# Optimization experiments

Measured on AMD Instinct MI355X. Metric: run time of the kernel, lower is better.

The kernel has to match this reference:

```python
import jax, jax.numpy as jnp
import numpy as np

B, L, D = 32, 256, 1024
ALIGN = 1024
FF = 2048
NUM_CLASSES = 3


def setup_inputs() -> dict:
    key = jax.random.key(0)
    ks = jax.random.split(key, 10)
    u = lambda k, shape: jax.random.uniform(k, shape, jnp.float32, -1.0, 1.0)
    return {
        "premises": jax.random.normal(ks[0], (B, L, D), jnp.float32),
        "hypotheses": jax.random.normal(ks[1], (B, L, D), jnp.float32),
        "W_F": u(ks[2], (D, ALIGN)),
        "W_G": u(ks[3], (2 * D, FF)),
        "W1": u(ks[4], (2 * FF, FF)) * 0.02,
        "b1": jnp.zeros((FF,), jnp.float32),
        "W2": u(ks[5], (FF, FF)) * 0.02,
        "b2": jnp.zeros((FF,), jnp.float32),
        "W3": u(ks[6], (FF, NUM_CLASSES)) * 0.02,
        "b3": jnp.zeros((NUM_CLASSES,), jnp.float32),
    }


def reference(premises, hypotheses, W_F, W_G, W1, b1, W2, b2, W3, b3):
    # ---- align: tanh-projected cross attention ----
    F_p = jnp.tanh(jnp.einsum("bpd,da->bpa", premises, W_F))      # [B,Lp,A]
    F_h = jnp.tanh(jnp.einsum("bhd,da->bha", hypotheses, W_F))    # [B,Lh,A]
    eijs = jnp.einsum("bpa,bha->bph", F_p, F_h)                   # [B,Lp,Lh]
    attn = jax.nn.softmax(eijs, axis=-1)                          # tf.nn.softmax: last axis
    betas = jnp.einsum("bph,bhd->bpd", attn, hypotheses)          # [B,Lp,D]
    alphas = jnp.einsum("bph,bpd->bhd", attn, premises)           # [B,Lh,D]

    # ---- compare (dropout is identity: p_keep = 1.0 at eval) ----
    V1 = jnp.tanh(jnp.concatenate([premises, betas], axis=2) @ W_G)    # [B,Lp,FF]
    V2 = jnp.tanh(jnp.concatenate([hypotheses, alphas], axis=2) @ W_G) # [B,Lh,FF]

    # ---- aggregate: sum-pool over sequence, concat ----
    agg = jnp.concatenate([V1.sum(axis=1), V2.sum(axis=1)], axis=1)    # [B,2*FF]

    # ---- classifier MLP ----
    a1 = jnp.tanh(agg @ W1 + b1)
    a2 = jnp.tanh(a1 @ W2 + b2)
    logits = a2 @ W3 + b3                                              # [B,3]
    return logits
```

## Files before the change

### kernel.cpp

```cpp
#include <hip/hip_runtime.h>
#include <hip/hip_bf16.h>
#include <stdint.h>


typedef __attribute__((ext_vector_type(8))) short    short8_t;
typedef __attribute__((ext_vector_type(4))) float    float4_t;
typedef __attribute__((ext_vector_type(8))) _Float16 half8_t;
typedef __attribute__((ext_vector_type(4))) _Float16 half4_t;

#define DEVI static __device__ __forceinline__

DEVI short f2bf(float f) {
  union { float f; unsigned u; } v; v.f = f;
  unsigned r = v.u + 0x7fffu + ((v.u >> 16) & 1u);
  return (short)(r >> 16);
}
DEVI float bf2f(short s) {
  union { unsigned u; float f; } v;
  v.u = ((unsigned)(unsigned short)s) << 16;
  return v.f;
}
DEVI void split2(float x, short& hi, short& lo) {
  hi = f2bf(x);
  lo = f2bf(x - bf2f(hi));
}
DEVI float fast_tanh(float x) {
  float e = __expf(2.0f * x);
  return 1.0f - 2.0f / (e + 1.0f);
}
DEVI void gload16(const void* g, void* l) {
  __builtin_amdgcn_global_load_lds(
      (const __attribute__((address_space(1))) void*)g,
      (__attribute__((address_space(3))) void*)l, 16, 0, 0);
}

template <int DO_TANH, int OUT_MODE>
__global__ __launch_bounds__(256) void gemm_nt_split(
    const short* __restrict__ Ah, const short* __restrict__ Al, int lda, long sA,
    const short* __restrict__ Bh, const short* __restrict__ Bl, int ldb, long sB,
    void* __restrict__ Ch, void* __restrict__ Cl, int ldc, long sC,
    int M, int K, int kslices)
{
  __shared__ __align__(16) short Ash[128][40];
  __shared__ __align__(16) short Asl[128][40];
  __shared__ __align__(16) short Bsh[128][40];
  __shared__ __align__(16) short Bsl[128][40];

  const int z  = blockIdx.z;
  const int zb = z / kslices;
  const int zk = z - zb * kslices;
  const int Ksub = K / kslices;
  const int kbeg = zk * Ksub, kend = kbeg + Ksub;

  Ah += (size_t)zb * sA;  Al += (size_t)zb * sA;
  Bh += (size_t)zb * sB;  Bl += (size_t)zb * sB;

  const int row0 = blockIdx.x * 128;
  const int col0 = blockIdx.y * 128;

  const int t    = threadIdx.x;
  const int lane = t & 63;
  const int wave = t >> 6;
  const int wr = wave >> 1, wc = wave & 1;
  const int m15 = lane & 15, q = lane >> 4;

  float4_t acc[4][4];
#pragma unroll
  for (int i = 0; i < 4; ++i)
#pragma unroll
    for (int j = 0; j < 4; ++j) acc[i][j] = (float4_t)0.0f;

  for (int k0 = kbeg; k0 < kend; k0 += 32) {
#pragma unroll
    for (int i = 0; i < 2; ++i) {
      int c  = t + 256 * i;
      int r  = c >> 2;
      int kc = (c & 3) << 3;
      size_t ao = (size_t)(row0 + r) * lda + k0 + kc;
      size_t bo = (size_t)(col0 + r) * ldb + k0 + kc;
      *(int4*)(&Ash[r][kc]) = *(const int4*)(Ah + ao);
      *(int4*)(&Asl[r][kc]) = *(const int4*)(Al + ao);
      *(int4*)(&Bsh[r][kc]) = *(const int4*)(Bh + bo);
      *(int4*)(&Bsl[r][kc]) = *(const int4*)(Bl + bo);
    }
    __syncthreads();

    short8_t ah[4], al[4];
#pragma unroll
    for (int i = 0; i < 4; ++i) {
      ah[i] = *(const short8_t*)(&Ash[wr * 64 + i * 16 + m15][q * 8]);
      al[i] = *(const short8_t*)(&Asl[wr * 64 + i * 16 + m15][q * 8]);
    }
#pragma unroll
    for (int j = 0; j < 4; ++j) {
      short8_t bh = *(const short8_t*)(&Bsh[wc * 64 + j * 16 + m15][q * 8]);
      short8_t bl = *(const short8_t*)(&Bsl[wc * 64 + j * 16 + m15][q * 8]);
#pragma unroll
      for (int i = 0; i < 4; ++i) {
        acc[i][j] = __builtin_amdgcn_mfma_f32_16x16x32_bf16(ah[i], bh, acc[i][j], 0, 0, 0);
        acc[i][j] = __builtin_amdgcn_mfma_f32_16x16x32_bf16(ah[i], bl, acc[i][j], 0, 0, 0);
        acc[i][j] = __builtin_amdgcn_mfma_f32_16x16x32_bf16(al[i], bh, acc[i][j], 0, 0, 0);
      }
    }
    __syncthreads();
  }

  short* Chs = (short*)Ch + (size_t)zb * sC;
  short* Cls = (short*)Cl + (size_t)zb * sC;
  float* Cf  = (float*)Ch + (size_t)zb * sC;
#pragma unroll
  for (int i = 0; i < 4; ++i) {
#pragma unroll
    for (int r = 0; r < 4; ++r) {
      int gm = row0 + wr * 64 + i * 16 + q * 4 + r;
      if (gm < M) {
#pragma unroll
        for (int j = 0; j < 4; ++j) {
          int gn = col0 + wc * 64 + j * 16 + m15;
          float v = acc[i][j][r];
          if (DO_TANH) v = fast_tanh(v);
          if (OUT_MODE == 0) {
            atomicAdd(&Cf[(size_t)gm * ldc + gn], v);
          } else {
            short hi, lo; split2(v, hi, lo);
            Chs[(size_t)gm * ldc + gn] = hi;
            Cls[(size_t)gm * ldc + gn] = lo;
          }
        }
      }
    }
  }
}

template <int MODE>
__global__ __launch_bounds__(256) void gemm_f16(
    const _Float16* __restrict__ A, int lda, long sA,
    const _Float16* __restrict__ B, int ldb, long sB,
    _Float16* __restrict__ C, int ldc, long sC,
    int K, float* __restrict__ agg)
{
  __shared__ __align__(16) _Float16 As[2 * 128 * 32];
  __shared__ __align__(16) _Float16 Bs[2 * 128 * 32];

  const int z = blockIdx.z;
  A += (size_t)z * sA;
  B += (size_t)z * sB;

  const int row0 = blockIdx.x * 128;
  const int col0 = blockIdx.y * 128;
  const int t = threadIdx.x, lane = t & 63, wave = t >> 6;
  const int wr = wave >> 1, wc = wave & 1;
  const int m15 = lane & 15, q = lane >> 4;

  const int srow = wave * 32 + (lane >> 2);
  const int cg   = ((lane & 3) ^ ((lane >> 3) & 3)) * 8;
  const _Float16* gA0 = A + (size_t)(row0 + srow) * lda + cg;
  const _Float16* gA1 = gA0 + (size_t)16 * lda;
  const _Float16* gB0 = B + (size_t)(col0 + srow) * ldb + cg;
  const _Float16* gB1 = gB0 + (size_t)16 * ldb;
  const _Float16* gA0b = gA0 + 32;
  const _Float16* gA1b = gA1 + 32;
  const _Float16* gB0b = gB0 + 32;
  const _Float16* gB1b = gB1 + 32;
  _Float16* lA0  = &As[(wave * 32) * 32];
  _Float16* lA1  = &As[(wave * 32 + 16) * 32];
  _Float16* lB0  = &Bs[(wave * 32) * 32];
  _Float16* lB1  = &Bs[(wave * 32 + 16) * 32];
  _Float16* lA0b = lA0 + 4096;
  _Float16* lA1b = lA1 + 4096;
  _Float16* lB0b = lB0 + 4096;
  _Float16* lB1b = lB1 + 4096;

  const int fs = (q ^ ((m15 >> 1) & 3)) * 8;
  int aoff[4], boff[4];
#pragma unroll
  for (int i = 0; i < 4; ++i) {
    aoff[i] = (wr * 64 + i * 16 + m15) * 32 + fs;
    boff[i] = (wc * 64 + i * 16 + m15) * 32 + fs;
  }

  float4_t acc[4][4];
#pragma unroll
  for (int i = 0; i < 4; ++i)
#pragma unroll
    for (int j = 0; j < 4; ++j) acc[i][j] = (float4_t)0.0f;

  for (int k0 = 0; k0 < K; k0 += 64) {
    gload16(gA0, lA0);  gload16(gA1, lA1);
    gload16(gB0, lB0);  gload16(gB1, lB1);
    gload16(gA0b, lA0b); gload16(gA1b, lA1b);
    gload16(gB0b, lB0b); gload16(gB1b, lB1b);
    gA0 += 64; gA1 += 64; gB0 += 64; gB1 += 64;
    gA0b += 64; gA1b += 64; gB0b += 64; gB1b += 64;
    __syncthreads();

#pragma unroll
    for (int h = 0; h < 2; ++h) {
      half8_t af[4], bfr[4];
#pragma unroll
      for (int i = 0; i < 4; ++i) af[i]  = *(const half8_t*)&As[h * 4096 + aoff[i]];
#pragma unroll
      for (int j = 0; j < 4; ++j) bfr[j] = *(const half8_t*)&Bs[h * 4096 + boff[j]];
#pragma unroll
      for (int i = 0; i < 4; ++i)
#pragma unroll
        for (int j = 0; j < 4; ++j)
          acc[i][j] = __builtin_amdgcn_mfma_f32_16x16x32_f16(af[i], bfr[j], acc[i][j], 0, 0, 0);
    }
    __syncthreads();
  }

  if (MODE == 2) {
    const int half_ = row0 >= 8192;
    const int b     = (row0 & 8191) >> 8;
#pragma unroll
    for (int j = 0; j < 4; ++j) {
      float s = 0.0f;
#pragma unroll
      for (int i = 0; i < 4; ++i)
#pragma unroll
        for (int r = 0; r < 4; ++r) s += fast_tanh(acc[i][j][r]);
      s += __shfl_xor(s, 16);
      s += __shfl_xor(s, 32);
      if (q == 0) {
        int col = col0 + wc * 64 + j * 16 + m15;
        atomicAdd(&agg[(size_t)b * 4096 + half_ * 2048 + col], s);
      }
    }
  } else {
    _Float16* Cp = C + (size_t)z * sC;
#pragma unroll
    for (int i = 0; i < 4; ++i)
#pragma unroll
      for (int r = 0; r < 4; ++r) {
        int gm = row0 + wr * 64 + i * 16 + q * 4 + r;
#pragma unroll
        for (int j = 0; j < 4; ++j) {
          int gn = col0 + wc * 64 + j * 16 + m15;
          Cp[(size_t)gm * ldc + gn] = (_Float16)acc[i][j][r];
        }
      }
  }
}

__global__ __launch_bounds__(256) void transpose_split(
    const float* __restrict__ in, short* __restrict__ oh, short* __restrict__ ol,
    int R, int C)
{
  __shared__ float tile[32][33];
  const int tx = threadIdx.x & 31, ty = threadIdx.x >> 5;
  const int c0 = blockIdx.x * 32, r0 = blockIdx.y * 32;
#pragma unroll
  for (int i = 0; i < 4; ++i) {
    int r = ty + i * 8;
    tile[r][tx] = in[(size_t)(r0 + r) * C + c0 + tx];
  }
  __syncthreads();
#pragma unroll
  for (int i = 0; i < 4; ++i) {
    int cc = ty + i * 8;
    float v = tile[tx][cc];
    short hi, lo; split2(v, hi, lo);
    size_t o = (size_t)(c0 + cc) * R + r0 + tx;
    oh[o] = hi;
    ol[o] = lo;
  }
}

__global__ __launch_bounds__(256) void transpose_f16(
    const float* __restrict__ in, _Float16* __restrict__ out, int R, int C)
{
  __shared__ float tile[32][33];
  const int tx = threadIdx.x & 31, ty = threadIdx.x >> 5;
  const int c0 = blockIdx.x * 32, r0 = blockIdx.y * 32;
#pragma unroll
  for (int i = 0; i < 4; ++i) {
    int r = ty + i * 8;
    tile[r][tx] = in[(size_t)(r0 + r) * C + c0 + tx];
  }
  __syncthreads();
#pragma unroll
  for (int i = 0; i < 4; ++i) {
    int cc = ty + i * 8;
    out[(size_t)(c0 + cc) * R + r0 + tx] = (_Float16)tile[tx][cc];
  }
}

__global__ __launch_bounds__(256) void transpose_f16_ph(
    const float* __restrict__ P, const float* __restrict__ Hh,
    _Float16* __restrict__ out)
{
  __shared__ float tile[32][33];
  const int zz = blockIdx.z;
  const float* in = (zz < 32 ? P : Hh) + (size_t)(zz & 31) * (256 * 1024);
  _Float16* o = out + (size_t)zz * (1024 * 256);
  const int tx = threadIdx.x & 31, ty = threadIdx.x >> 5;
  const int c0 = blockIdx.x * 32, r0 = blockIdx.y * 32;
#pragma unroll
  for (int i = 0; i < 4; ++i) {
    int r = ty + i * 8;
    tile[r][tx] = in[(size_t)(r0 + r) * 1024 + c0 + tx];
  }
  __syncthreads();
#pragma unroll
  for (int i = 0; i < 4; ++i) {
    int cc = ty + i * 8;
    o[(size_t)(c0 + cc) * 256 + r0 + tx] = (_Float16)tile[tx][cc];
  }
}

__global__ __launch_bounds__(256) void transpose_b2b(
    const short* __restrict__ in, short* __restrict__ out,
    int R, int C, long sIn, long sOut)
{
  __shared__ short tile[32][33];
  in  += (size_t)blockIdx.z * sIn;
  out += (size_t)blockIdx.z * sOut;
  const int tx = threadIdx.x & 31, ty = threadIdx.x >> 5;
  const int c0 = blockIdx.x * 32, r0 = blockIdx.y * 32;
#pragma unroll
  for (int i = 0; i < 4; ++i) {
    int r = ty + i * 8;
    tile[r][tx] = in[(size_t)(r0 + r) * C + c0 + tx];
  }
  __syncthreads();
#pragma unroll
  for (int i = 0; i < 4; ++i) {
    int cc = ty + i * 8;
    out[(size_t)(c0 + cc) * R + r0 + tx] = tile[tx][cc];
  }
}

__global__ __launch_bounds__(256) void conv_in(
    const float* __restrict__ P, const float* __restrict__ Hh,
    short* __restrict__ oh, short* __restrict__ ol, _Float16* __restrict__ cat)
{
  const int zz = blockIdx.z;
  const float* in = zz ? Hh : P;
  oh  += (size_t)zz * 8192 * 1024;
  ol  += (size_t)zz * 8192 * 1024;
  cat += (size_t)zz * 8192 * 2048;
  size_t i = ((size_t)blockIdx.x * 256 + threadIdx.x) * 4;
  float4 v = *(const float4*)&in[i];
  short4 h, l;
  split2(v.x, h.x, l.x); split2(v.y, h.y, l.y);
  split2(v.z, h.z, l.z); split2(v.w, h.w, l.w);
  *(short4*)&oh[i] = h;
  *(short4*)&ol[i] = l;
  size_t row = i >> 10;
  int col    = (int)(i & 1023);
  half4_t c16;
  c16.x = (_Float16)v.x; c16.y = (_Float16)v.y;
  c16.z = (_Float16)v.z; c16.w = (_Float16)v.w;
  *(half4_t*)&cat[row * 2048 + col] = c16;
}

__global__ __launch_bounds__(256) void conv_split(
    const float* __restrict__ in, short* __restrict__ oh, short* __restrict__ ol,
    int n)
{
  int i = (blockIdx.x * 256 + threadIdx.x) * 4;
  if (i < n) {
    float4 v = *(const float4*)&in[i];
    short4 h, l;
    split2(v.x, h.x, l.x); split2(v.y, h.y, l.y);
    split2(v.z, h.z, l.z); split2(v.w, h.w, l.w);
    *(short4*)&oh[i] = h;
    *(short4*)&ol[i] = l;
  }
}

__global__ __launch_bounds__(256) void zero_f32(float* __restrict__ p, int n)
{
  int i = blockIdx.x * 256 + threadIdx.x;
  if (i < n) p[i] = 0.0f;
}

__global__ __launch_bounds__(256) void softmax_rows(
    const float* __restrict__ e, _Float16* __restrict__ attn)
{
  const int row  = blockIdx.x * 4 + (threadIdx.x >> 6);
  const int lane = threadIdx.x & 63;
  const float4 v = *(const float4*)&e[(size_t)row * 256 + lane * 4];
  float m = fmaxf(fmaxf(v.x, v.y), fmaxf(v.z, v.w));
#pragma unroll
  for (int off = 32; off; off >>= 1) m = fmaxf(m, __shfl_xor(m, off));
  float e0 = __expf(v.x - m), e1 = __expf(v.y - m);
  float e2 = __expf(v.z - m), e3 = __expf(v.w - m);
  float s = e0 + e1 + e2 + e3;
#pragma unroll
  for (int off = 32; off; off >>= 1) s += __shfl_xor(s, off);
  float inv = 1.0f / s;
  half4_t o;
  o.x = (_Float16)(e0 * inv); o.y = (_Float16)(e1 * inv);
  o.z = (_Float16)(e2 * inv); o.w = (_Float16)(e3 * inv);
  *(half4_t*)&attn[(size_t)row * 256 + lane * 4] = o;
}

__global__ __launch_bounds__(256) void bias_tanh_split(
    const float* __restrict__ c, const float* __restrict__ bias,
    short* __restrict__ oh, short* __restrict__ ol, int n)
{
  int i = blockIdx.x * 256 + threadIdx.x;
  if (i < n) {
    float v = fast_tanh(c[i] + bias[i & 2047]);
    short hi, lo; split2(v, hi, lo);
    oh[i] = hi;
    ol[i] = lo;
  }
}

__global__ __launch_bounds__(256) void logits2(
    const float* __restrict__ c2f, const float* __restrict__ b2,
    const float* __restrict__ W3, const float* __restrict__ b3,
    float* __restrict__ out)
{
  const int b = blockIdx.x, t = threadIdx.x;
  float p0 = 0.f, p1 = 0.f, p2 = 0.f;
  for (int k = t; k < 2048; k += 256) {
    float a = fast_tanh(c2f[b * 2048 + k] + b2[k]);
    p0 += a * W3[k * 3 + 0];
    p1 += a * W3[k * 3 + 1];
    p2 += a * W3[k * 3 + 2];
  }
#pragma unroll
  for (int off = 32; off; off >>= 1) {
    p0 += __shfl_xor(p0, off);
    p1 += __shfl_xor(p1, off);
    p2 += __shfl_xor(p2, off);
  }
  __shared__ float red[4][3];
  if ((t & 63) == 0) {
    red[t >> 6][0] = p0; red[t >> 6][1] = p1; red[t >> 6][2] = p2;
  }
  __syncthreads();
  if (t < 3) out[b * 3 + t] = b3[t] + red[0][t] + red[1][t] + red[2][t] + red[3][t];
}

extern "C" void kernel_launch(void* const* d_in, const int* in_sizes, int n_in,
                              void* d_out, int out_size, void* d_ws, size_t ws_size,
                              hipStream_t stream) {
  (void)in_sizes; (void)n_in; (void)out_size; (void)ws_size;
  const float* P   = (const float*)d_in[0];
  const float* H   = (const float*)d_in[1];
  const float* W_F = (const float*)d_in[2];
  const float* W_G = (const float*)d_in[3];
  const float* W1  = (const float*)d_in[4];
  const float* b1  = (const float*)d_in[5];
  const float* W2  = (const float*)d_in[6];
  const float* b2  = (const float*)d_in[7];
  const float* W3  = (const float*)d_in[8];
  const float* b3  = (const float*)d_in[9];
  float* out = (float*)d_out;

  char* wsp = (char*)d_ws;
  auto alloc = [&](size_t bytes) {
    char* p = wsp;
    wsp += (bytes + 255) & ~(size_t)255;
    return p;
  };
  short*    Pp_h  = (short*)alloc(16384ull * 1024 * 2);
  short*    Pp_l  = (short*)alloc(16384ull * 1024 * 2);
  _Float16* Cat16 = (_Float16*)alloc(16384ull * 2048 * 2);
  short*    Fbuf  = (short*)alloc(32ull * 1024 * 1024 * 2);
  short*    WFT_h = (short*)alloc(1024ull * 1024 * 2);
  short*    WFT_l = (short*)alloc(1024ull * 1024 * 2);
  _Float16* WGT16 = (_Float16*)alloc(2048ull * 2048 * 2);
  float*    eijs  = (float*)alloc(32ull * 256 * 256 * 4);
  _Float16* attn  = (_Float16*)alloc(32ull * 256 * 256 * 2);
  _Float16* attnT = (_Float16*)alloc(32ull * 256 * 256 * 2);
  float*    agg   = (float*)alloc(32ull * 4096 * 4);
  short*    aggb_h= (short*)alloc(128ull * 4096 * 2);
  short*    aggb_l= (short*)alloc(128ull * 4096 * 2);
  float*    c1f   = (float*)alloc(32ull * 2048 * 4);
  float*    c2f   = (float*)alloc(32ull * 2048 * 4);
  short*    a1_h  = (short*)alloc(128ull * 2048 * 2);
  short*    a1_l  = (short*)alloc(128ull * 2048 * 2);

  short* F_h = Fbuf;
  short* F_l = Fbuf + 16384ull * 1024;
  _Float16* PHbT = (_Float16*)Fbuf;
  _Float16* PbT  = PHbT;
  _Float16* HbT  = PHbT + 32ull * 1024 * 256;
  short* W1T_h = Fbuf;
  short* W1T_l = Fbuf +  8ull * 1024 * 1024;
  short* W2T_h = Fbuf + 16ull * 1024 * 1024;
  short* W2T_l = Fbuf + 20ull * 1024 * 1024;

  conv_in<<<dim3(8192, 1, 2), 256, 0, stream>>>(P, H, Pp_h, Pp_l, Cat16);
  transpose_split<<<dim3(32, 32, 1), 256, 0, stream>>>(W_F, WFT_h, WFT_l, 1024, 1024);
  transpose_f16<<<dim3(64, 64, 1), 256, 0, stream>>>(W_G, WGT16, 2048, 2048);

  gemm_nt_split<1, 1><<<dim3(128, 8, 1), 256, 0, stream>>>(
      Pp_h, Pp_l, 1024, 0, WFT_h, WFT_l, 1024, 0,
      F_h, F_l, 1024, 0, 16384, 1024, 1);

  zero_f32<<<8192, 256, 0, stream>>>(eijs, 32 * 256 * 256);
  gemm_nt_split<0, 0><<<dim3(2, 2, 128), 256, 0, stream>>>(
      F_h, F_l, 1024, 256 * 1024,
      F_h + 8192ull * 1024, F_l + 8192ull * 1024, 1024, 256 * 1024,
      eijs, nullptr, 256, 65536, 256, 1024, 4);

  softmax_rows<<<2048, 256, 0, stream>>>(eijs, attn);
  transpose_b2b<<<dim3(8, 8, 32), 256, 0, stream>>>(
      (const short*)attn, (short*)attnT, 256, 256, 65536, 65536);
  transpose_f16_ph<<<dim3(32, 8, 64), 256, 0, stream>>>(P, H, PHbT);

  gemm_f16<1><<<dim3(2, 8, 32), 256, 0, stream>>>(
      attn, 256, 65536, HbT, 256, 1024 * 256,
      Cat16 + 1024, 2048, 256 * 2048, 256, nullptr);
  gemm_f16<1><<<dim3(2, 8, 32), 256, 0, stream>>>(
      attnT, 256, 65536, PbT, 256, 1024 * 256,
      Cat16 + 8192ull * 2048 + 1024, 2048, 256 * 2048, 256, nullptr);

  zero_f32<<<512, 256, 0, stream>>>(agg, 32 * 4096);
  gemm_f16<2><<<dim3(128, 16, 1), 256, 0, stream>>>(
      Cat16, 2048, 0, WGT16, 2048, 0, nullptr, 0, 0, 2048, agg);

  transpose_split<<<dim3(64, 128, 1), 256, 0, stream>>>(W1, W1T_h, W1T_l, 4096, 2048);
  transpose_split<<<dim3(64, 64, 1),  256, 0, stream>>>(W2, W2T_h, W2T_l, 2048, 2048);
  conv_split<<<128, 256, 0, stream>>>(agg, aggb_h, aggb_l, 32 * 4096);
  zero_f32<<<256, 256, 0, stream>>>(c1f, 32 * 2048);
  gemm_nt_split<0, 0><<<dim3(1, 16, 8), 256, 0, stream>>>(
      aggb_h, aggb_l, 4096, 0, W1T_h, W1T_l, 4096, 0,
      c1f, nullptr, 2048, 0, 32, 4096, 8);
  bias_tanh_split<<<256, 256, 0, stream>>>(c1f, b1, a1_h, a1_l, 32 * 2048);
  zero_f32<<<256, 256, 0, stream>>>(c2f, 32 * 2048);
  gemm_nt_split<0, 0><<<dim3(1, 16, 4), 256, 0, stream>>>(
      a1_h, a1_l, 2048, 0, W2T_h, W2T_l, 2048, 0,
      c2f, nullptr, 2048, 0, 32, 2048, 4);
  logits2<<<32, 256, 0, stream>>>(c2f, b2, W3, b3, out);
}
```

Baseline: 643.0 us.

## Replace compare GEMM with 256x256-tile, 8-wave pipelined kernel with fused tanh-sum

Adds a dedicated kernel for the large compare GEMM (16384x2048x2048) that uses 256x256 block tiles with 8 waves, double-buffered LDS, XOR-swizzled direct global-to-LDS loads, and a staged schedule interleaving loads with MFMA phases under raised wave priority. The tanh and sequence-sum epilogue with atomic accumulation into agg is kept. The aim is more operand reuse per LDS load and better overlap of memory traffic with matrix math than the old 128x128 tile kernel. The risks are higher register and LDS pressure (128 KB LDS per block) and fewer blocks in flight.

```diff
diff --git a/kernel.cpp b/kernel.cpp
--- a/kernel.cpp
+++ b/kernel.cpp
@@ -210,24 +210,7 @@
     __syncthreads();
   }
 
-  if (MODE == 2) {
-    const int half_ = row0 >= 8192;
-    const int b     = (row0 & 8191) >> 8;
-#pragma unroll
-    for (int j = 0; j < 4; ++j) {
-      float s = 0.0f;
-#pragma unroll
-      for (int i = 0; i < 4; ++i)
-#pragma unroll
-        for (int r = 0; r < 4; ++r) s += fast_tanh(acc[i][j][r]);
-      s += __shfl_xor(s, 16);
-      s += __shfl_xor(s, 32);
-      if (q == 0) {
-        int col = col0 + wc * 64 + j * 16 + m15;
-        atomicAdd(&agg[(size_t)b * 4096 + half_ * 2048 + col], s);
-      }
-    }
-  } else {
+  {
     _Float16* Cp = C + (size_t)z * sC;
 #pragma unroll
     for (int i = 0; i < 4; ++i)
@@ -240,6 +223,170 @@
           Cp[(size_t)gm * ldc + gn] = (_Float16)acc[i][j][r];
         }
       }
+  }
+}
+
+__global__ __launch_bounds__(512, 2) void gemm_f16_sum8(
+    const _Float16* __restrict__ A, int lda,
+    const _Float16* __restrict__ B, int ldb,
+    int K, float* __restrict__ agg)
+{
+  __shared__ __align__(16) _Float16 As[2][256 * 64];
+  __shared__ __align__(16) _Float16 Bs[2][256 * 64];
+
+  const int row0 = blockIdx.x * 256;
+  const int col0 = blockIdx.y * 256;
+  const int tid  = threadIdx.x;
+  const int lane = tid & 63, wave = tid >> 6;
+  const int wr = wave >> 2, wc = wave & 3;
+  const int m15 = lane & 15, q = lane >> 4;
+  const int nt = K / 64;
+
+  const int srow = wave * 16 + (lane >> 3);
+  const int cg   = ((lane & 7) ^ ((lane >> 3) & 7)) * 8;
+  const _Float16* gAh[2] = {
+      A + (size_t)(row0 +       srow) * lda + cg,
+      A + (size_t)(row0 + 128 + srow) * lda + cg };
+  const _Float16* gBh[2] = {
+      B + (size_t)(col0 +       srow) * ldb + cg,
+      B + (size_t)(col0 + 128 + srow) * ldb + cg };
+  _Float16* lA[2][2]; _Float16* lB[2][2];
+#pragma unroll
+  for (int bb = 0; bb < 2; ++bb)
+#pragma unroll
+    for (int h = 0; h < 2; ++h) {
+      lA[bb][h] = &As[bb][(h * 128 + wave * 16) * 64];
+      lB[bb][h] = &Bs[bb][(h * 128 + wave * 16) * 64];
+    }
+  auto stage = [&](const _Float16* gb, int ld, _Float16* l, int kt) {
+    const _Float16* g = gb + kt * 64;
+    gload16(g, l);
+    gload16(g + 8 * (size_t)ld, l + 512);
+  };
+
+  const int x0 = ( q      ^ (m15 & 7)) * 8;
+  const int x1 = ((4 | q) ^ (m15 & 7)) * 8;
+
+  float4_t acc[8][4];
+#pragma unroll
+  for (int i = 0; i < 8; ++i)
+#pragma unroll
+    for (int j = 0; j < 4; ++j) acc[i][j] = (float4_t)0.0f;
+  half8_t aM0[4][2], aM1[4][2], bN0[2][2], bN1[2][2];
+
+  stage(gAh[0], lda, lA[0][0], 0);
+  stage(gAh[1], lda, lA[0][1], 0);
+  stage(gBh[0], ldb, lB[0][0], 0);
+  stage(gBh[1], ldb, lB[0][1], 0);
+  stage(gAh[0], lda, lA[1][0], 1);
+  stage(gAh[1], lda, lA[1][1], 1);
+  asm volatile("s_waitcnt vmcnt(4)" ::: "memory");
+  asm volatile("s_barrier" ::: "memory");
+
+  for (int t = 0; t < nt; ++t) {
+    const int cur = t & 1, nxt = cur ^ 1;
+
+#pragma unroll
+    for (int i = 0; i < 4; ++i) {
+      const int ra = (wr * 128 + i * 16 + m15) * 64;
+      aM0[i][0] = *(const half8_t*)&As[cur][ra + x0];
+      aM0[i][1] = *(const half8_t*)&As[cur][ra + x1];
+    }
+#pragma unroll
+    for (int j = 0; j < 2; ++j) {
+      const int rb = (wc * 64 + j * 16 + m15) * 64;
+      bN0[j][0] = *(const half8_t*)&Bs[cur][rb + x0];
+      bN0[j][1] = *(const half8_t*)&Bs[cur][rb + x1];
+    }
+    if (t + 1 < nt) stage(gBh[0], ldb, lB[nxt][0], t + 1);
+    asm volatile("s_barrier" ::: "memory");
+    asm volatile("s_waitcnt lgkmcnt(0)" ::: "memory");
+    __builtin_amdgcn_sched_barrier(0);
+    __builtin_amdgcn_s_setprio(1);
+#pragma unroll
+    for (int i = 0; i < 4; ++i)
+#pragma unroll
+      for (int j = 0; j < 2; ++j) {
+        acc[i][j] = __builtin_amdgcn_mfma_f32_16x16x32_f16(aM0[i][0], bN0[j][0], acc[i][j], 0, 0, 0);
+        acc[i][j] = __builtin_amdgcn_mfma_f32_16x16x32_f16(aM0[i][1], bN0[j][1], acc[i][j], 0, 0, 0);
+      }
+    __builtin_amdgcn_s_setprio(0);
+    asm volatile("s_barrier" ::: "memory");
+
+#pragma unroll
+    for (int i = 0; i < 4; ++i) {
+      const int ra = (wr * 128 + (4 + i) * 16 + m15) * 64;
+      aM1[i][0] = *(const half8_t*)&As[cur][ra + x0];
+      aM1[i][1] = *(const half8_t*)&As[cur][ra + x1];
+    }
+#pragma unroll
+    for (int j = 0; j < 2; ++j) {
+      const int rb = (wc * 64 + (2 + j) * 16 + m15) * 64;
+      bN1[j][0] = *(const half8_t*)&Bs[cur][rb + x0];
+      bN1[j][1] = *(const half8_t*)&Bs[cur][rb + x1];
+    }
+    if (t + 1 < nt) stage(gBh[1], ldb, lB[nxt][1], t + 1);
+    asm volatile("s_barrier" ::: "memory");
+    asm volatile("s_waitcnt lgkmcnt(0)" ::: "memory");
+    __builtin_amdgcn_sched_barrier(0);
+    __builtin_amdgcn_s_setprio(1);
+#pragma unroll
+    for (int i = 0; i < 4; ++i)
+#pragma unroll
+      for (int j = 0; j < 2; ++j) {
+        acc[i][2 + j] = __builtin_amdgcn_mfma_f32_16x16x32_f16(aM0[i][0], bN1[j][0], acc[i][2 + j], 0, 0, 0);
+        acc[i][2 + j] = __builtin_amdgcn_mfma_f32_16x16x32_f16(aM0[i][1], bN1[j][1], acc[i][2 + j], 0, 0, 0);
+      }
+    __builtin_amdgcn_s_setprio(0);
+    asm volatile("s_barrier" ::: "memory");
+
+    if (t + 2 < nt) stage(gAh[0], lda, lA[cur][0], t + 2);
+    asm volatile("s_barrier" ::: "memory");
+    __builtin_amdgcn_s_setprio(1);
+#pragma unroll
+    for (int i = 0; i < 4; ++i)
+#pragma unroll
+      for (int j = 0; j < 2; ++j) {
+        acc[4 + i][j] = __builtin_amdgcn_mfma_f32_16x16x32_f16(aM1[i][0], bN0[j][0], acc[4 + i][j], 0, 0, 0);
+        acc[4 + i][j] = __builtin_amdgcn_mfma_f32_16x16x32_f16(aM1[i][1], bN0[j][1], acc[4 + i][j], 0, 0, 0);
+      }
+    __builtin_amdgcn_s_setprio(0);
+    asm volatile("s_barrier" ::: "memory");
+
+    if (t + 2 < nt) stage(gAh[1], lda, lA[cur][1], t + 2);
+    asm volatile("s_barrier" ::: "memory");
+    __builtin_amdgcn_s_setprio(1);
+#pragma unroll
+    for (int i = 0; i < 4; ++i)
+#pragma unroll
+      for (int j = 0; j < 2; ++j) {
+        acc[4 + i][2 + j] = __builtin_amdgcn_mfma_f32_16x16x32_f16(aM1[i][0], bN1[j][0], acc[4 + i][2 + j], 0, 0, 0);
+        acc[4 + i][2 + j] = __builtin_amdgcn_mfma_f32_16x16x32_f16(aM1[i][1], bN1[j][1], acc[4 + i][2 + j], 0, 0, 0);
+      }
+    __builtin_amdgcn_s_setprio(0);
+    if (t + 2 < nt) {
+      asm volatile("s_waitcnt vmcnt(4)" ::: "memory");
+    } else if (t + 1 < nt) {
+      asm volatile("s_waitcnt vmcnt(0)" ::: "memory");
+    }
+    asm volatile("s_barrier" ::: "memory");
+  }
+
+  const int half_ = row0 >= 8192;
+  const int b     = (row0 & 8191) >> 8;
+#pragma unroll
+  for (int j = 0; j < 4; ++j) {
+    float s = 0.0f;
+#pragma unroll
+    for (int i = 0; i < 8; ++i)
+#pragma unroll
+      for (int r = 0; r < 4; ++r) s += fast_tanh(acc[i][j][r]);
+    s += __shfl_xor(s, 16);
+    s += __shfl_xor(s, 32);
+    if (q == 0) {
+      int col = col0 + wc * 64 + j * 16 + m15;
+      atomicAdd(&agg[(size_t)b * 4096 + half_ * 2048 + col], s);
+    }
   }
 }
 
@@ -514,8 +661,8 @@
       Cat16 + 8192ull * 2048 + 1024, 2048, 256 * 2048, 256, nullptr);
 
   zero_f32<<<512, 256, 0, stream>>>(agg, 32 * 4096);
-  gemm_f16<2><<<dim3(128, 16, 1), 256, 0, stream>>>(
-      Cat16, 2048, 0, WGT16, 2048, 0, nullptr, 0, 0, 2048, agg);
+  gemm_f16_sum8<<<dim3(64, 8, 1), 512, 0, stream>>>(
+      Cat16, 2048, WGT16, 2048, 2048, agg);
 
   transpose_split<<<dim3(64, 128, 1), 256, 0, stream>>>(W1, W1T_h, W1T_l, 4096, 2048);
   transpose_split<<<dim3(64, 64, 1),  256, 0, stream>>>(W2, W2T_h, W2T_l, 2048, 2048);
```

Result: faster. 627.6 us (-2.4%).

## Add 256x256-tile 8-wave pipelined GEMM with fused tanh-sum for compare stage

Applied to the files above, without the earlier changes.

Replaces the MODE 2 path of the generic 128x128 gemm_f16 with a dedicated kernel for the big compare GEMM (16384x2048x2048). It uses 256x256 tiles across 8 waves, a 4-slot LDS ring with async global-to-LDS loads issued two steps ahead, a swizzled LDS layout, and raised MFMA issue priority. The fused tanh plus sequence-sum epilogue with atomicAdd into agg is kept. The goal is more data reuse per tile, fewer atomics and better overlap of loads with MFMA. The cost is higher register and LDS pressure and only 512 blocks.

```diff
diff --git a/kernel.cpp b/kernel.cpp
--- a/kernel.cpp
+++ b/kernel.cpp
@@ -210,24 +210,7 @@
     __syncthreads();
   }
 
-  if (MODE == 2) {
-    const int half_ = row0 >= 8192;
-    const int b     = (row0 & 8191) >> 8;
-#pragma unroll
-    for (int j = 0; j < 4; ++j) {
-      float s = 0.0f;
-#pragma unroll
-      for (int i = 0; i < 4; ++i)
-#pragma unroll
-        for (int r = 0; r < 4; ++r) s += fast_tanh(acc[i][j][r]);
-      s += __shfl_xor(s, 16);
-      s += __shfl_xor(s, 32);
-      if (q == 0) {
-        int col = col0 + wc * 64 + j * 16 + m15;
-        atomicAdd(&agg[(size_t)b * 4096 + half_ * 2048 + col], s);
-      }
-    }
-  } else {
+  {
     _Float16* Cp = C + (size_t)z * sC;
 #pragma unroll
     for (int i = 0; i < 4; ++i)
@@ -240,6 +223,113 @@
           Cp[(size_t)gm * ldc + gn] = (_Float16)acc[i][j][r];
         }
       }
+  }
+}
+
+__global__ __launch_bounds__(512, 2) void gemm_f16_sum8(
+    const _Float16* __restrict__ A, int lda,
+    const _Float16* __restrict__ B, int ldb,
+    int K, float* __restrict__ agg)
+{
+  __shared__ __align__(16) _Float16 LDS[4][2 * 256 * 32];
+
+  const int row0 = blockIdx.x * 256;
+  const int col0 = blockIdx.y * 256;
+  const int tid  = threadIdx.x;
+  const int lane = tid & 63, wave = tid >> 6;
+  const int wr = wave >> 2, wc = wave & 3;
+  const int m15 = lane & 15, q = lane >> 4;
+  const int nt = K / 32;
+
+  const int srow = wave * 32 + (lane >> 2);
+  const int cg   = ((lane & 3) ^ ((lane >> 2) & 3)) * 8;
+  const _Float16* gA = A + (size_t)(row0 + srow) * lda + cg;
+  const _Float16* gB = B + (size_t)(col0 + srow) * ldb + cg;
+
+  auto stageA = [&](int t) {
+    const _Float16* g = gA + t * 32;
+    _Float16* l = &LDS[t & 3][wave * 1024];
+    gload16(g, l);
+    gload16(g + (size_t)16 * lda, l + 512);
+  };
+  auto stageB = [&](int t) {
+    const _Float16* g = gB + t * 32;
+    _Float16* l = &LDS[t & 3][8192 + wave * 1024];
+    gload16(g, l);
+    gload16(g + (size_t)16 * ldb, l + 512);
+  };
+
+  const int xq = (q ^ (m15 & 3)) * 8;
+  int aoff[8], boff[4];
+#pragma unroll
+  for (int i = 0; i < 8; ++i)
+    aoff[i] = (wr * 128 + i * 16 + m15) * 32 + xq;
+#pragma unroll
+  for (int j = 0; j < 4; ++j)
+    boff[j] = 8192 + (wc * 64 + j * 16 + m15) * 32 + xq;
+
+  float4_t acc[8][4];
+#pragma unroll
+  for (int i = 0; i < 8; ++i)
+#pragma unroll
+    for (int j = 0; j < 4; ++j) acc[i][j] = (float4_t)0.0f;
+
+  stageA(0); stageB(0);
+  stageA(1); stageB(1);
+  asm volatile("s_waitcnt vmcnt(4)");
+  __builtin_amdgcn_s_barrier();
+
+  for (int t = 0; t < nt; ++t) {
+    const _Float16* buf = &LDS[t & 3][0];
+    __builtin_amdgcn_sched_barrier(0);
+
+    half8_t a0[4], a1[4], bb[4];
+#pragma unroll
+    for (int i = 0; i < 4; ++i) a0[i] = *(const half8_t*)&buf[aoff[i]];
+#pragma unroll
+    for (int j = 0; j < 4; ++j) bb[j] = *(const half8_t*)&buf[boff[j]];
+#pragma unroll
+    for (int i = 0; i < 4; ++i) a1[i] = *(const half8_t*)&buf[aoff[4 + i]];
+
+    if (t + 2 < nt) { stageA(t + 2); stageB(t + 2); }
+
+    __builtin_amdgcn_s_setprio(1);
+#pragma unroll
+    for (int i = 0; i < 4; ++i)
+#pragma unroll
+      for (int j = 0; j < 4; ++j)
+        acc[i][j] = __builtin_amdgcn_mfma_f32_16x16x32_f16(a0[i], bb[j], acc[i][j], 0, 0, 0);
+#pragma unroll
+    for (int i = 0; i < 4; ++i)
+#pragma unroll
+      for (int j = 0; j < 4; ++j)
+        acc[4 + i][j] = __builtin_amdgcn_mfma_f32_16x16x32_f16(a1[i], bb[j], acc[4 + i][j], 0, 0, 0);
+    __builtin_amdgcn_s_setprio(0);
+
+    __builtin_amdgcn_sched_barrier(0);
+    if (t + 2 < nt) {
+      asm volatile("s_waitcnt vmcnt(4)");
+    } else if (t + 1 < nt) {
+      asm volatile("s_waitcnt vmcnt(0)");
+    }
+    __builtin_amdgcn_s_barrier();
+  }
+
+  const int half_ = row0 >= 8192;
+  const int b     = (row0 & 8191) >> 8;
+#pragma unroll
+  for (int j = 0; j < 4; ++j) {
+    float s = 0.0f;
+#pragma unroll
+    for (int i = 0; i < 8; ++i)
+#pragma unroll
+      for (int r = 0; r < 4; ++r) s += fast_tanh(acc[i][j][r]);
+    s += __shfl_xor(s, 16);
+    s += __shfl_xor(s, 32);
+    if (q == 0) {
+      int col = col0 + wc * 64 + j * 16 + m15;
+      atomicAdd(&agg[(size_t)b * 4096 + half_ * 2048 + col], s);
+    }
   }
 }
 
@@ -514,8 +604,8 @@
       Cat16 + 8192ull * 2048 + 1024, 2048, 256 * 2048, 256, nullptr);
 
   zero_f32<<<512, 256, 0, stream>>>(agg, 32 * 4096);
-  gemm_f16<2><<<dim3(128, 16, 1), 256, 0, stream>>>(
-      Cat16, 2048, 0, WGT16, 2048, 0, nullptr, 0, 0, 2048, agg);
+  gemm_f16_sum8<<<dim3(64, 8, 1), 512, 0, stream>>>(
+      Cat16, 2048, WGT16, 2048, 2048, agg);
 
   transpose_split<<<dim3(64, 128, 1), 256, 0, stream>>>(W1, W1T_h, W1T_l, 4096, 2048);
   transpose_split<<<dim3(64, 64, 1),  256, 0, stream>>>(W2, W2T_h, W2T_l, 2048, 2048);
```

Result: faster. 610.2 us (-5.1%).
